# Performance work log

Hardware: AMD Instinct MI355X
Metric: run time of the kernel (lower is better)

The kernel has to match this reference:

```python
import jax, jax.numpy as jnp
from jax import lax
import numpy as np

NODE = 100000
D = 256      # input_dim
H = 256      # hidden_dim
P = 4096     # num paths between the pair
L = 8        # path length (hops)
OUT = 1


def setup_inputs() -> dict:
    key = jax.random.key(0)
    ks = jax.random.split(key, 10)
    s = 1.0 / np.sqrt(H)
    return {
        "embedding": jax.random.normal(ks[0], (NODE, D), jnp.float32) * 0.1,
        "w_ih": jax.random.normal(ks[1], (4 * H, D), jnp.float32) * s,
        "w_hh": jax.random.normal(ks[2], (4 * H, H), jnp.float32) * s,
        "b_ih": jax.random.normal(ks[3], (4 * H,), jnp.float32) * s,
        "b_hh": jax.random.normal(ks[4], (4 * H,), jnp.float32) * s,
        "w_lin": jax.random.normal(ks[5], (OUT, H + 2 * D), jnp.float32) * 0.05,
        "b_lin": jax.random.normal(ks[6], (OUT,), jnp.float32) * 0.05,
        "paths": jax.random.randint(ks[7], (P, L), 0, NODE, jnp.int64),
        "user_id": jax.random.randint(ks[8], (1,), 0, NODE, jnp.int64),
        "item_id": jax.random.randint(ks[9], (1,), 0, NODE, jnp.int64),
    }


def _lstm_final_hidden(x, w_ih, w_hh, b_ih, b_hh):
    # x: [P, L, D] -> final hidden state h_n: [P, H] (PyTorch gate order i,f,g,o)
    p, _, _ = x.shape
    h = x.shape  # noqa (shape comment)
    hidden = w_hh.shape[1]
    b = b_ih + b_hh

    def step(carry, x_t):
        h, c = carry
        gates = x_t @ w_ih.T + h @ w_hh.T + b  # [P, 4H]
        i, f, g, o = jnp.split(gates, 4, axis=-1)
        c = jax.nn.sigmoid(f) * c + jax.nn.sigmoid(i) * jnp.tanh(g)
        h = jax.nn.sigmoid(o) * jnp.tanh(c)
        return (h, c), None

    h0 = jnp.zeros((p, hidden), x.dtype)
    c0 = jnp.zeros((p, hidden), x.dtype)
    (h_n, _), _ = lax.scan(step, (h0, c0), jnp.swapaxes(x, 0, 1))  # scan over L
    return h_n


def reference(embedding, w_ih, w_hh, b_ih, b_hh, w_lin, b_lin, paths, user_id, item_id):
    # Batched version of the per-path loop: embed all paths, one LSTM scan.
    x = embedding[paths]                                   # [P, L, D]
    sum_hidden = _lstm_final_hidden(x, w_ih, w_hh, b_ih, b_hh)  # [P, H] (== stacked h_n)

    # MaxPool2d((1, H)) over hidden dim -> attention logits over paths
    att = jnp.max(sum_hidden, axis=-1, keepdims=True)      # [P, 1]
    att = jax.nn.softmax(att, axis=0)                      # softmax over paths
    path_emb = jnp.sum(sum_hidden * att, axis=0, keepdims=True)  # [1, H]

    user_emb = embedding[user_id]                          # [1, D]
    item_emb = embedding[item_id]                          # [1, D]
    emb = jnp.concatenate([user_emb, item_emb, path_emb], axis=-1)  # [1, 2D+H]
    out = jax.nn.sigmoid(emb @ w_lin.T + b_lin)            # [1, OUT]
    return out
```

## Files before the change

kernel.cpp:

```cpp
#include <hip/hip_runtime.h>
#include <stdint.h>

#define NPATHS 4096
#define LPATH  8
#define DIM    256
#define HID    256

typedef short  short4v __attribute__((ext_vector_type(4)));
typedef short  short8v __attribute__((ext_vector_type(8)));
typedef float  float4v __attribute__((ext_vector_type(4)));

__device__ __forceinline__ unsigned short f2bf(float f) {
    union { float f; uint32_t u; } v; v.f = f;
    uint32_t u = v.u;
    u += 0x7FFFu + ((u >> 16) & 1u);
    return (unsigned short)(u >> 16);
}
__device__ __forceinline__ float bf2f(unsigned short s) {
    return __uint_as_float(((uint32_t)s) << 16);
}
__device__ __forceinline__ float fast_sigmoid(float x) {
    return 1.0f / (1.0f + __expf(-x));
}
__device__ __forceinline__ float fast_tanh(float x) {
    x = fminf(15.0f, fmaxf(-15.0f, x));
    float e = __expf(2.0f * x);
    return (e - 1.0f) / (e + 1.0f);
}
__device__ __forceinline__ unsigned int encf(float f) {
    unsigned int u = __float_as_uint(f);
    return (u & 0x80000000u) ? ~u : (u | 0x80000000u);
}
__device__ __forceinline__ float decf(unsigned int u) {
    return (u & 0x80000000u) ? __uint_as_float(u & 0x7FFFFFFFu) : __uint_as_float(~u);
}

__device__ __forceinline__ void dma16(void* lds, const void* g) {
    typedef const unsigned int __attribute__((address_space(1)))* gp_t;
    typedef unsigned int __attribute__((address_space(3)))* lp_t;
    gp_t gp = reinterpret_cast<gp_t>(reinterpret_cast<uintptr_t>(g));
    lp_t lp = reinterpret_cast<lp_t>(static_cast<unsigned int>(reinterpret_cast<uintptr_t>(lds)));
    __builtin_amdgcn_global_load_lds(gp, lp, 16, 0, 0);
}

__global__ void prep_gather(const float* __restrict__ w_ih, const float* __restrict__ w_hh,
                            const float* __restrict__ b_ih, const float* __restrict__ b_hh,
                            const float* __restrict__ embedding, const int* __restrict__ paths,
                            unsigned short* __restrict__ WfB, float* __restrict__ bias,
                            unsigned int* __restrict__ logits_enc, float* __restrict__ path_emb,
                            unsigned short* __restrict__ Xb) {
    int bid = blockIdx.x;
    if (bid < 512) {
        int gid  = bid * 256 + threadIdx.x;
        int base = gid * 4;
        int j0   = base & 31;
        int unit = (base >> 5) & 255;
        int gkc  = base >> 13;
        int g    = gkc >> 4, kc = gkc & 15;
        int row  = g * 256 + unit;
        int k    = kc * 32 + j0;
        const float* src = (k < DIM) ? (w_ih + (size_t)row * DIM + k)
                                     : (w_hh + (size_t)row * HID + (k - DIM));
        float4 v = *(const float4*)src;
        short4v pk = {(short)f2bf(v.x), (short)f2bf(v.y), (short)f2bf(v.z), (short)f2bf(v.w)};
        *(short4v*)(WfB + base) = pk;
        if (gid < 1024) bias[gid] = b_ih[gid] + b_hh[gid];
        if (gid < NPATHS) logits_enc[gid] = 0u;
        if (gid < 256) path_emb[gid] = 0.0f;
    } else {
        int gid  = (bid - 512) * 256 + threadIdx.x;
        int rowt = gid >> 6;
        int seg  = gid & 63;
        int p    = rowt & (NPATHS - 1);
        int t    = rowt >> 12;
        int node = paths[p * LPATH + t];
        float4 v = *(const float4*)(embedding + (size_t)node * DIM + seg * 4);
        short4v pk = {(short)f2bf(v.x), (short)f2bf(v.y), (short)f2bf(v.z), (short)f2bf(v.w)};
        *(short4v*)(Xb + (size_t)rowt * DIM + seg * 4) = pk;
    }
}

template<bool FIRST, bool LAST>
__global__ __launch_bounds__(256, 1)
void step_kernel(const unsigned short* __restrict__ Xb,
                 const unsigned short* __restrict__ WfB,
                 const float* __restrict__ bias,
                 const unsigned short* __restrict__ h_in,
                 unsigned short* __restrict__ h_out,
                 float* __restrict__ c_g,
                 unsigned int* __restrict__ logits_enc,
                 int t) {
    __shared__ __align__(16) short sA[64 * 512];
    short* hT = sA;

    const int tid   = threadIdx.x;
    const int wave  = tid >> 6;
    const int lane  = tid & 63;
    const int l15   = lane & 15;
    const int quad  = lane >> 4;
    const int blk   = blockIdx.x;
    const int ptile = blk & 63;
    const int utile = blk >> 6;
    const int p0    = ptile * 64;
    const int u0    = utile * 64;

    {
        const char* xpl = (const char*)Xb + ((size_t)t * NPATHS + p0) * 512;
        const char* hpl = (const char*)h_in + (size_t)p0 * 512;
        const char* xl  = xpl + l15 * 512 + quad * 16;
        const char* hl  = hpl + l15 * 512 + quad * 16;
#pragma unroll
        for (int m = 0; m < 16; ++m) {
            int rf = m >> 2, kq = m & 3;
            if (FIRST && kq >= 2) continue;
            int fp = rf * 16 + kq * 4 + wave;
            const char* base = (kq < 2) ? xl : hl;
            int kk = ((kq & 1) * 4 + wave) * 64;
            dma16(sA + fp * 512, base + rf * 8192 + kk);
        }
    }

    short8v Bf[4][16];
    float bb[4];
    const int unit = u0 + wave * 16 + l15;
#pragma unroll
    for (int g = 0; g < 4; ++g) {
        bb[g] = bias[g * 256 + unit];
#pragma unroll
        for (int kc = 0; kc < 16; ++kc)
            Bf[g][kc] = *(const short8v*)(WfB + (((g * 16 + kc) * 256 + unit) * 32 + quad * 8));
    }

    __syncthreads();

    float4v acc[4][4];
    const float4v z4 = {0.0f, 0.0f, 0.0f, 0.0f};
#pragma unroll
    for (int rf = 0; rf < 4; ++rf)
#pragma unroll
        for (int g = 0; g < 4; ++g) acc[rf][g] = z4;

    auto kstep = [&](int kc) {
#pragma unroll
        for (int rf = 0; rf < 4; ++rf) {
            short8v a = *(const short8v*)(sA + ((rf * 16 + kc) << 9) + lane * 8);
#pragma unroll
            for (int g = 0; g < 4; ++g)
                acc[rf][g] = __builtin_amdgcn_mfma_f32_16x16x32_bf16(
                    a, Bf[g][kc], acc[rf][g], 0, 0, 0);
        }
    };
    if (FIRST) {
#pragma unroll
        for (int kc = 0; kc < 8; ++kc) kstep(kc);
    } else {
#pragma unroll
        for (int kc = 0; kc < 16; ++kc) kstep(kc);
    }

    float hv[16];
#pragma unroll
    for (int rf = 0; rf < 4; ++rf) {
#pragma unroll
        for (int r = 0; r < 4; ++r) {
            int row = rf * 16 + quad * 4 + r;
            int idx = rf * 4 + r;
            float iv = acc[rf][0][r] + bb[0];
            float fv = acc[rf][1][r] + bb[1];
            float gv = acc[rf][2][r] + bb[2];
            float ov = acc[rf][3][r] + bb[3];
            size_t coff = (size_t)(p0 + row) * HID + unit;
            float cp = FIRST ? 0.0f : c_g[coff];
            float cn = fast_sigmoid(fv) * cp + fast_sigmoid(iv) * fast_tanh(gv);
            if (!LAST) c_g[coff] = cn;
            hv[idx] = fast_sigmoid(ov) * fast_tanh(cn);
        }
    }

    __syncthreads();
#pragma unroll
    for (int rf = 0; rf < 4; ++rf)
#pragma unroll
        for (int r = 0; r < 4; ++r)
            hT[(rf * 16 + quad * 4 + r) * 72 + wave * 16 + l15] =
                (short)f2bf(hv[rf * 4 + r]);
    __syncthreads();
    {
        unsigned short* hdst = h_out + (size_t)p0 * HID + u0;
#pragma unroll
        for (int i = 0; i < 2; ++i) {
            int cid = i * 256 + tid;
            int row = cid >> 3, seg = cid & 7;
            short8v v = *(const short8v*)(hT + row * 72 + seg * 8);
            *(short8v*)(hdst + (size_t)row * HID + seg * 8) = v;
        }
    }

    if (LAST) {
#pragma unroll
        for (int idx = 0; idx < 16; ++idx) {
            float m = hv[idx];
            m = fmaxf(m, __shfl_xor(m, 1, 64));
            m = fmaxf(m, __shfl_xor(m, 2, 64));
            m = fmaxf(m, __shfl_xor(m, 4, 64));
            m = fmaxf(m, __shfl_xor(m, 8, 64));
            if (l15 == 0) {
                int rf = idx >> 2, r = idx & 3;
                atomicMax(&logits_enc[p0 + rf * 16 + quad * 4 + r], encf(m));
            }
        }
    }
}

__global__ void attn_sum_kernel(const unsigned short* __restrict__ h_final,
                                const unsigned int* __restrict__ enc,
                                float* __restrict__ path_emb) {
    __shared__ float red[256];
    __shared__ float wts[16];
    int tid = threadIdx.x;
    int p0  = blockIdx.x * 16;

    float vals[16];
    float m = -1e30f;
#pragma unroll
    for (int i = 0; i < 16; ++i) {
        vals[i] = decf(enc[i * 256 + tid]);
        m = fmaxf(m, vals[i]);
    }
    red[tid] = m; __syncthreads();
    for (int s = 128; s > 0; s >>= 1) {
        if (tid < s) red[tid] = fmaxf(red[tid], red[tid + s]);
        __syncthreads();
    }
    m = red[0]; __syncthreads();
    float sum = 0.0f;
#pragma unroll
    for (int i = 0; i < 16; ++i) sum += __expf(vals[i] - m);
    red[tid] = sum; __syncthreads();
    for (int s = 128; s > 0; s >>= 1) {
        if (tid < s) red[tid] += red[tid + s];
        __syncthreads();
    }
    if (tid == 0) red[0] = 1.0f / red[0];
    __syncthreads();
    float invZ = red[0];
    if (tid < 16) wts[tid] = __expf(decf(enc[p0 + tid]) - m) * invZ;
    __syncthreads();

    float acc = 0.0f;
#pragma unroll
    for (int j = 0; j < 16; ++j)
        acc += wts[j] * bf2f(h_final[(size_t)(p0 + j) * HID + tid]);
    atomicAdd(&path_emb[tid], acc);
}

__global__ void final_kernel(const float* __restrict__ embedding,
                             const int* __restrict__ user_id,
                             const int* __restrict__ item_id,
                             const float* __restrict__ w_lin,
                             const float* __restrict__ b_lin,
                             const float* __restrict__ path_emb,
                             float* __restrict__ out) {
    __shared__ float red[256];
    int tid = threadIdx.x;
    int u  = user_id[0];
    int it = item_id[0];
    float s = w_lin[tid]       * embedding[(size_t)u  * DIM + tid]
            + w_lin[256 + tid] * embedding[(size_t)it * DIM + tid]
            + w_lin[512 + tid] * path_emb[tid];
    red[tid] = s; __syncthreads();
    for (int st = 128; st > 0; st >>= 1) {
        if (tid < st) red[tid] += red[tid + st];
        __syncthreads();
    }
    if (tid == 0) out[0] = 1.0f / (1.0f + __expf(-(red[0] + b_lin[0])));
}

extern "C" void kernel_launch(void* const* d_in, const int* in_sizes, int n_in,
                              void* d_out, int out_size, void* d_ws, size_t ws_size,
                              hipStream_t stream) {
    const float* embedding = (const float*)d_in[0];
    const float* w_ih      = (const float*)d_in[1];
    const float* w_hh      = (const float*)d_in[2];
    const float* b_ih      = (const float*)d_in[3];
    const float* b_hh      = (const float*)d_in[4];
    const float* w_lin     = (const float*)d_in[5];
    const float* b_lin     = (const float*)d_in[6];
    const int*   paths     = (const int*)d_in[7];
    const int*   user_id   = (const int*)d_in[8];
    const int*   item_id   = (const int*)d_in[9];
    float* outp = (float*)d_out;

    char* ws = (char*)d_ws;
    size_t off = 0;
    auto alloc = [&](size_t n) { void* p = ws + off; off = (off + n + 255) & ~(size_t)255; return p; };
    unsigned short* WfB       = (unsigned short*)alloc((size_t)1024 * 512 * 2);
    float*          bias      = (float*)alloc(1024 * 4);
    unsigned int*   logits_enc= (unsigned int*)alloc(NPATHS * 4);
    float*          path_emb  = (float*)alloc(HID * 4);
    unsigned short* Xb        = (unsigned short*)alloc((size_t)LPATH * NPATHS * DIM * 2);
    unsigned short* h_buf     = (unsigned short*)alloc((size_t)2 * NPATHS * HID * 2);
    float*          c_g       = (float*)alloc((size_t)NPATHS * HID * 4);

    prep_gather<<<8704, 256, 0, stream>>>(w_ih, w_hh, b_ih, b_hh, embedding, paths,
                                          WfB, bias, logits_enc, path_emb, Xb);

    for (int t = 0; t < LPATH; ++t) {
        const unsigned short* hin = h_buf + (size_t)(t & 1) * NPATHS * HID;
        unsigned short*      hout = h_buf + (size_t)((t + 1) & 1) * NPATHS * HID;
        if (t == 0)
            step_kernel<true, false><<<256, 256, 0, stream>>>(Xb, WfB, bias, hin, hout,
                                                              c_g, logits_enc, t);
        else if (t == LPATH - 1)
            step_kernel<false, true><<<256, 256, 0, stream>>>(Xb, WfB, bias, hin, hout,
                                                              c_g, logits_enc, t);
        else
            step_kernel<false, false><<<256, 256, 0, stream>>>(Xb, WfB, bias, hin, hout,
                                                               c_g, logits_enc, t);
    }

    attn_sum_kernel<<<NPATHS / 16, 256, 0, stream>>>(h_buf, logits_enc, path_emb);
    final_kernel<<<1, 256, 0, stream>>>(embedding, user_id, item_id, w_lin, b_lin,
                                        path_emb, outp);
}
```

Baseline: 274.3 us.

## Fuse next-step embedding gather into LSTM step kernel and stream weight fragments

The prep kernel now gathers only the t=0 embeddings. Each step kernel gathers and bf16-packs the embeddings for step t+1 itself, overlapping that latency with the MFMA work and cutting the separate large gather launch. Weight fragments are now streamed four k-chunks ahead instead of all being preloaded into registers. The h_in DMA and c-state loads are issued after the x part starts, so loads overlap compute. In exchange the step kernel grows in complexity, adds an extra barrier, and uses a separate LDS buffer for the transposed h output.

```diff
diff --git a/kernel.cpp b/kernel.cpp
--- a/kernel.cpp
+++ b/kernel.cpp
@@ -41,6 +41,15 @@
     gp_t gp = reinterpret_cast<gp_t>(reinterpret_cast<uintptr_t>(g));
     lp_t lp = reinterpret_cast<lp_t>(static_cast<unsigned int>(reinterpret_cast<uintptr_t>(lds)));
     __builtin_amdgcn_global_load_lds(gp, lp, 16, 0, 0);
+}
+
+__device__ __forceinline__ short8v pack8(float4 a, float4 b) {
+    short8v r;
+    r[0] = (short)f2bf(a.x); r[1] = (short)f2bf(a.y);
+    r[2] = (short)f2bf(a.z); r[3] = (short)f2bf(a.w);
+    r[4] = (short)f2bf(b.x); r[5] = (short)f2bf(b.y);
+    r[6] = (short)f2bf(b.z); r[7] = (short)f2bf(b.w);
+    return r;
 }
 
 __global__ void prep_gather(const float* __restrict__ w_ih, const float* __restrict__ w_hh,
@@ -68,30 +77,35 @@
         if (gid < NPATHS) logits_enc[gid] = 0u;
         if (gid < 256) path_emb[gid] = 0.0f;
     } else {
-        int gid  = (bid - 512) * 256 + threadIdx.x;
-        int rowt = gid >> 6;
-        int seg  = gid & 63;
-        int p    = rowt & (NPATHS - 1);
-        int t    = rowt >> 12;
-        int node = paths[p * LPATH + t];
-        float4 v = *(const float4*)(embedding + (size_t)node * DIM + seg * 4);
-        short4v pk = {(short)f2bf(v.x), (short)f2bf(v.y), (short)f2bf(v.z), (short)f2bf(v.w)};
-        *(short4v*)(Xb + (size_t)rowt * DIM + seg * 4) = pk;
+        int sb   = bid - 512;
+        int row  = (sb & 63) * 64 + (sb >> 6) * 16 + (threadIdx.x >> 4);
+        int c0   = (threadIdx.x & 15) * 16;
+        int node = paths[row * LPATH];
+        const float* src = embedding + (size_t)node * DIM + c0;
+        float4 g0 = *(const float4*)(src + 0);
+        float4 g1 = *(const float4*)(src + 4);
+        float4 g2 = *(const float4*)(src + 8);
+        float4 g3 = *(const float4*)(src + 12);
+        unsigned short* xd = Xb + (size_t)row * 256 + c0;
+        *(short8v*)(xd)     = pack8(g0, g1);
+        *(short8v*)(xd + 8) = pack8(g2, g3);
     }
 }
 
 template<bool FIRST, bool LAST>
 __global__ __launch_bounds__(256, 1)
-void step_kernel(const unsigned short* __restrict__ Xb,
+void step_kernel(unsigned short* __restrict__ Xb,
                  const unsigned short* __restrict__ WfB,
                  const float* __restrict__ bias,
                  const unsigned short* __restrict__ h_in,
                  unsigned short* __restrict__ h_out,
                  float* __restrict__ c_g,
                  unsigned int* __restrict__ logits_enc,
+                 const float* __restrict__ embedding,
+                 const int* __restrict__ paths,
                  int t) {
     __shared__ __align__(16) short sA[64 * 512];
-    short* hT = sA;
+    __shared__ __align__(16) short hTb[64 * 72];
 
     const int tid   = threadIdx.x;
     const int wave  = tid >> 6;
@@ -103,35 +117,61 @@
     const int utile = blk >> 6;
     const int p0    = ptile * 64;
     const int u0    = utile * 64;
+    const int unit  = u0 + wave * 16 + l15;
 
     {
-        const char* xpl = (const char*)Xb + ((size_t)t * NPATHS + p0) * 512;
-        const char* hpl = (const char*)h_in + (size_t)p0 * 512;
-        const char* xl  = xpl + l15 * 512 + quad * 16;
-        const char* hl  = hpl + l15 * 512 + quad * 16;
-#pragma unroll
-        for (int m = 0; m < 16; ++m) {
-            int rf = m >> 2, kq = m & 3;
-            if (FIRST && kq >= 2) continue;
+        const char* xl = (const char*)Xb + ((size_t)t * NPATHS + p0) * 512
+                       + l15 * 512 + quad * 16;
+#pragma unroll
+        for (int m = 0; m < 8; ++m) {
+            int rf = m >> 1, kq = m & 1;
             int fp = rf * 16 + kq * 4 + wave;
-            const char* base = (kq < 2) ? xl : hl;
-            int kk = ((kq & 1) * 4 + wave) * 64;
-            dma16(sA + fp * 512, base + rf * 8192 + kk);
-        }
-    }
-
-    short8v Bf[4][16];
+            dma16(sA + fp * 512, xl + rf * 8192 + (kq * 4 + wave) * 64);
+        }
+    }
+
+    short8v Bs[4][4];
     float bb[4];
-    const int unit = u0 + wave * 16 + l15;
-#pragma unroll
-    for (int g = 0; g < 4; ++g) {
-        bb[g] = bias[g * 256 + unit];
-#pragma unroll
-        for (int kc = 0; kc < 16; ++kc)
-            Bf[g][kc] = *(const short8v*)(WfB + (((g * 16 + kc) * 256 + unit) * 32 + quad * 8));
-    }
-
-    __syncthreads();
+    auto loadB = [&](int kc) {
+#pragma unroll
+        for (int g = 0; g < 4; ++g)
+            Bs[g][kc & 3] = *(const short8v*)(WfB + (((g * 16 + kc) * 256 + unit) * 32 + quad * 8));
+    };
+#pragma unroll
+    for (int g = 0; g < 4; ++g) bb[g] = bias[g * 256 + unit];
+#pragma unroll
+    for (int kc = 0; kc < 4; ++kc) loadB(kc);
+
+    __syncthreads();
+
+    if (!FIRST) {
+        const char* hl = (const char*)h_in + (size_t)p0 * 512 + l15 * 512 + quad * 16;
+#pragma unroll
+        for (int m = 0; m < 8; ++m) {
+            int rf = m >> 1, kq = m & 1;
+            int fp = rf * 16 + 8 + kq * 4 + wave;
+            dma16(sA + fp * 512, hl + rf * 8192 + (kq * 4 + wave) * 64);
+        }
+    }
+
+    float4 gvf[4];
+    int grow = 0;
+    if (!LAST) {
+        grow = p0 + utile * 16 + (tid >> 4);
+        int node = paths[grow * LPATH + (t + 1)];
+        const float* src = embedding + (size_t)node * DIM + (tid & 15) * 16;
+#pragma unroll
+        for (int i = 0; i < 4; ++i) gvf[i] = *(const float4*)(src + i * 4);
+    }
+
+    float cpre[16];
+    if (!FIRST) {
+#pragma unroll
+        for (int rf = 0; rf < 4; ++rf)
+#pragma unroll
+            for (int r = 0; r < 4; ++r)
+                cpre[rf * 4 + r] = c_g[(size_t)(p0 + rf * 16 + quad * 4 + r) * HID + unit];
+    }
 
     float4v acc[4][4];
     const float4v z4 = {0.0f, 0.0f, 0.0f, 0.0f};
@@ -147,15 +187,26 @@
 #pragma unroll
             for (int g = 0; g < 4; ++g)
                 acc[rf][g] = __builtin_amdgcn_mfma_f32_16x16x32_bf16(
-                    a, Bf[g][kc], acc[rf][g], 0, 0, 0);
+                    a, Bs[g][kc & 3], acc[rf][g], 0, 0, 0);
         }
     };
-    if (FIRST) {
-#pragma unroll
-        for (int kc = 0; kc < 8; ++kc) kstep(kc);
-    } else {
-#pragma unroll
-        for (int kc = 0; kc < 16; ++kc) kstep(kc);
+
+#pragma unroll
+    for (int kc = 0; kc < 8; ++kc) {
+        kstep(kc);
+        int nk = kc + 4;
+        if (nk < (FIRST ? 8 : 16)) loadB(nk);
+    }
+
+    __syncthreads();
+
+    if (!FIRST) {
+#pragma unroll
+        for (int kc = 8; kc < 16; ++kc) {
+            kstep(kc);
+            int nk = kc + 4;
+            if (nk < 16) loadB(nk);
+        }
     }
 
     float hv[16];
@@ -167,22 +218,26 @@
             int idx = rf * 4 + r;
             float iv = acc[rf][0][r] + bb[0];
             float fv = acc[rf][1][r] + bb[1];
-            float gv = acc[rf][2][r] + bb[2];
+            float gg = acc[rf][2][r] + bb[2];
             float ov = acc[rf][3][r] + bb[3];
-            size_t coff = (size_t)(p0 + row) * HID + unit;
-            float cp = FIRST ? 0.0f : c_g[coff];
-            float cn = fast_sigmoid(fv) * cp + fast_sigmoid(iv) * fast_tanh(gv);
-            if (!LAST) c_g[coff] = cn;
+            float cp = FIRST ? 0.0f : cpre[idx];
+            float cn = fast_sigmoid(fv) * cp + fast_sigmoid(iv) * fast_tanh(gg);
+            if (!LAST) c_g[(size_t)(p0 + row) * HID + unit] = cn;
             hv[idx] = fast_sigmoid(ov) * fast_tanh(cn);
         }
     }
 
-    __syncthreads();
+    if (!LAST) {
+        unsigned short* xd = Xb + ((size_t)(t + 1) * NPATHS + grow) * 256 + (tid & 15) * 16;
+        *(short8v*)(xd)     = pack8(gvf[0], gvf[1]);
+        *(short8v*)(xd + 8) = pack8(gvf[2], gvf[3]);
+    }
+
 #pragma unroll
     for (int rf = 0; rf < 4; ++rf)
 #pragma unroll
         for (int r = 0; r < 4; ++r)
-            hT[(rf * 16 + quad * 4 + r) * 72 + wave * 16 + l15] =
+            hTb[(rf * 16 + quad * 4 + r) * 72 + wave * 16 + l15] =
                 (short)f2bf(hv[rf * 4 + r]);
     __syncthreads();
     {
@@ -191,7 +246,7 @@
         for (int i = 0; i < 2; ++i) {
             int cid = i * 256 + tid;
             int row = cid >> 3, seg = cid & 7;
-            short8v v = *(const short8v*)(hT + row * 72 + seg * 8);
+            short8v v = *(const short8v*)(hTb + row * 72 + seg * 8);
             *(short8v*)(hdst + (size_t)row * HID + seg * 8) = v;
         }
     }
@@ -302,21 +357,24 @@
     unsigned short* h_buf     = (unsigned short*)alloc((size_t)2 * NPATHS * HID * 2);
     float*          c_g       = (float*)alloc((size_t)NPATHS * HID * 4);
 
-    prep_gather<<<8704, 256, 0, stream>>>(w_ih, w_hh, b_ih, b_hh, embedding, paths,
-                                          WfB, bias, logits_enc, path_emb, Xb);
+    prep_gather<<<768, 256, 0, stream>>>(w_ih, w_hh, b_ih, b_hh, embedding, paths,
+                                         WfB, bias, logits_enc, path_emb, Xb);
 
     for (int t = 0; t < LPATH; ++t) {
         const unsigned short* hin = h_buf + (size_t)(t & 1) * NPATHS * HID;
         unsigned short*      hout = h_buf + (size_t)((t + 1) & 1) * NPATHS * HID;
         if (t == 0)
             step_kernel<true, false><<<256, 256, 0, stream>>>(Xb, WfB, bias, hin, hout,
-                                                              c_g, logits_enc, t);
+                                                              c_g, logits_enc,
+                                                              embedding, paths, t);
         else if (t == LPATH - 1)
             step_kernel<false, true><<<256, 256, 0, stream>>>(Xb, WfB, bias, hin, hout,
-                                                              c_g, logits_enc, t);
+                                                              c_g, logits_enc,
+                                                              embedding, paths, t);
         else
             step_kernel<false, false><<<256, 256, 0, stream>>>(Xb, WfB, bias, hin, hout,
-                                                               c_g, logits_enc, t);
+                                                               c_g, logits_enc,
+                                                               embedding, paths, t);
     }
 
     attn_sum_kernel<<<NPATHS / 16, 256, 0, stream>>>(h_buf, logits_enc, path_emb);
```

New measurement: 266.4 us. 1.03x faster.

## Fuse all LSTM timesteps and the embedding gather into one persistent kernel

Applied to the files above, without the earlier changes.

Replaces the separate gather pass and eight per-timestep launches with a single kernel. Each block owns 16 paths for all 8 steps, keeping the cell state in registers and the hidden state in swizzled LDS, and gathers the next step's embeddings while the current step computes. The final attention reduction and output layer are merged into one kernel that uses a completion counter, and the encoded atomicMax logits are replaced by a direct per-path write. In exchange, every block now streams the whole bf16 weight matrix from global memory on every step, since the weights are no longer kept resident in registers.

```diff
diff --git a/kernel.cpp b/kernel.cpp
--- a/kernel.cpp
+++ b/kernel.cpp
@@ -27,196 +27,212 @@
     float e = __expf(2.0f * x);
     return (e - 1.0f) / (e + 1.0f);
 }
-__device__ __forceinline__ unsigned int encf(float f) {
-    unsigned int u = __float_as_uint(f);
-    return (u & 0x80000000u) ? ~u : (u | 0x80000000u);
-}
-__device__ __forceinline__ float decf(unsigned int u) {
-    return (u & 0x80000000u) ? __uint_as_float(u & 0x7FFFFFFFu) : __uint_as_float(~u);
-}
-
-__device__ __forceinline__ void dma16(void* lds, const void* g) {
-    typedef const unsigned int __attribute__((address_space(1)))* gp_t;
-    typedef unsigned int __attribute__((address_space(3)))* lp_t;
-    gp_t gp = reinterpret_cast<gp_t>(reinterpret_cast<uintptr_t>(g));
-    lp_t lp = reinterpret_cast<lp_t>(static_cast<unsigned int>(reinterpret_cast<uintptr_t>(lds)));
-    __builtin_amdgcn_global_load_lds(gp, lp, 16, 0, 0);
-}
-
-__global__ void prep_gather(const float* __restrict__ w_ih, const float* __restrict__ w_hh,
+
+__global__ void prep_kernel(const float* __restrict__ w_ih, const float* __restrict__ w_hh,
                             const float* __restrict__ b_ih, const float* __restrict__ b_hh,
-                            const float* __restrict__ embedding, const int* __restrict__ paths,
                             unsigned short* __restrict__ WfB, float* __restrict__ bias,
-                            unsigned int* __restrict__ logits_enc, float* __restrict__ path_emb,
-                            unsigned short* __restrict__ Xb) {
-    int bid = blockIdx.x;
-    if (bid < 512) {
-        int gid  = bid * 256 + threadIdx.x;
-        int base = gid * 4;
-        int j0   = base & 31;
-        int unit = (base >> 5) & 255;
-        int gkc  = base >> 13;
-        int g    = gkc >> 4, kc = gkc & 15;
-        int row  = g * 256 + unit;
-        int k    = kc * 32 + j0;
-        const float* src = (k < DIM) ? (w_ih + (size_t)row * DIM + k)
-                                     : (w_hh + (size_t)row * HID + (k - DIM));
-        float4 v = *(const float4*)src;
-        short4v pk = {(short)f2bf(v.x), (short)f2bf(v.y), (short)f2bf(v.z), (short)f2bf(v.w)};
-        *(short4v*)(WfB + base) = pk;
-        if (gid < 1024) bias[gid] = b_ih[gid] + b_hh[gid];
-        if (gid < NPATHS) logits_enc[gid] = 0u;
-        if (gid < 256) path_emb[gid] = 0.0f;
-    } else {
-        int gid  = (bid - 512) * 256 + threadIdx.x;
-        int rowt = gid >> 6;
-        int seg  = gid & 63;
-        int p    = rowt & (NPATHS - 1);
-        int t    = rowt >> 12;
-        int node = paths[p * LPATH + t];
-        float4 v = *(const float4*)(embedding + (size_t)node * DIM + seg * 4);
-        short4v pk = {(short)f2bf(v.x), (short)f2bf(v.y), (short)f2bf(v.z), (short)f2bf(v.w)};
-        *(short4v*)(Xb + (size_t)rowt * DIM + seg * 4) = pk;
-    }
-}
-
-template<bool FIRST, bool LAST>
-__global__ __launch_bounds__(256, 1)
-void step_kernel(const unsigned short* __restrict__ Xb,
-                 const unsigned short* __restrict__ WfB,
-                 const float* __restrict__ bias,
-                 const unsigned short* __restrict__ h_in,
-                 unsigned short* __restrict__ h_out,
-                 float* __restrict__ c_g,
-                 unsigned int* __restrict__ logits_enc,
-                 int t) {
-    __shared__ __align__(16) short sA[64 * 512];
-    short* hT = sA;
-
-    const int tid   = threadIdx.x;
-    const int wave  = tid >> 6;
-    const int lane  = tid & 63;
-    const int l15   = lane & 15;
-    const int quad  = lane >> 4;
-    const int blk   = blockIdx.x;
-    const int ptile = blk & 63;
-    const int utile = blk >> 6;
-    const int p0    = ptile * 64;
-    const int u0    = utile * 64;
+                            float* __restrict__ path_emb, unsigned int* __restrict__ done) {
+    int gid  = blockIdx.x * 256 + threadIdx.x;
+    int base = gid * 4;
+    int j0   = base & 31;
+    int unit = (base >> 5) & 255;
+    int gkc  = base >> 13;
+    int g    = gkc >> 4, kc = gkc & 15;
+    int row  = g * 256 + unit;
+    int k    = kc * 32 + j0;
+    const float* src = (k < DIM) ? (w_ih + (size_t)row * DIM + k)
+                                 : (w_hh + (size_t)row * HID + (k - DIM));
+    float4 v = *(const float4*)src;
+    short4v pk = {(short)f2bf(v.x), (short)f2bf(v.y), (short)f2bf(v.z), (short)f2bf(v.w)};
+    *(short4v*)(WfB + base) = pk;
+    if (gid < 1024) bias[gid] = b_ih[gid] + b_hh[gid];
+    if (gid < 256)  path_emb[gid] = 0.0f;
+    if (gid == 0)   *done = 0u;
+}
+
+__global__ __launch_bounds__(512, 2)
+void mega_kernel(const float* __restrict__ embedding, const int* __restrict__ paths,
+                 const unsigned short* __restrict__ WfB, const float* __restrict__ bias,
+                 unsigned short* __restrict__ h_final, float* __restrict__ logits) {
+    __shared__ __align__(16) short sAx[2][8 * 512];
+    __shared__ __align__(16) short h_lds[16 * 256];
+    __shared__ float red[16 * 8];
+
+    const int tid  = threadIdx.x;
+    const int w    = tid >> 6;
+    const int lane = tid & 63;
+    const int l15  = lane & 15;
+    const int quad = lane >> 4;
+    const int p0   = blockIdx.x * 16;
+    const int unitA = w * 32 + l15;
+    const int unitB = unitA + 16;
+    const int boffA = unitA * 32 + quad * 8;
+    const int boffB = unitB * 32 + quad * 8;
+
+    float bb[4][2];
+#pragma unroll
+    for (int g = 0; g < 4; ++g) {
+        bb[g][0] = bias[g * 256 + unitA];
+        bb[g][1] = bias[g * 256 + unitB];
+    }
 
     {
-        const char* xpl = (const char*)Xb + ((size_t)t * NPATHS + p0) * 512;
-        const char* hpl = (const char*)h_in + (size_t)p0 * 512;
-        const char* xl  = xpl + l15 * 512 + quad * 16;
-        const char* hl  = hpl + l15 * 512 + quad * 16;
-#pragma unroll
-        for (int m = 0; m < 16; ++m) {
-            int rf = m >> 2, kq = m & 3;
-            if (FIRST && kq >= 2) continue;
-            int fp = rf * 16 + kq * 4 + wave;
-            const char* base = (kq < 2) ? xl : hl;
-            int kk = ((kq & 1) * 4 + wave) * 64;
-            dma16(sA + fp * 512, base + rf * 8192 + kk);
-        }
-    }
-
-    short8v Bf[4][16];
-    float bb[4];
-    const int unit = u0 + wave * 16 + l15;
-#pragma unroll
-    for (int g = 0; g < 4; ++g) {
-        bb[g] = bias[g * 256 + unit];
-#pragma unroll
-        for (int kc = 0; kc < 16; ++kc)
-            Bf[g][kc] = *(const short8v*)(WfB + (((g * 16 + kc) * 256 + unit) * 32 + quad * 8));
-    }
-
-    __syncthreads();
-
-    float4v acc[4][4];
-    const float4v z4 = {0.0f, 0.0f, 0.0f, 0.0f};
-#pragma unroll
-    for (int rf = 0; rf < 4; ++rf)
-#pragma unroll
-        for (int g = 0; g < 4; ++g) acc[rf][g] = z4;
-
-    auto kstep = [&](int kc) {
-#pragma unroll
-        for (int rf = 0; rf < 4; ++rf) {
-            short8v a = *(const short8v*)(sA + ((rf * 16 + kc) << 9) + lane * 8);
-#pragma unroll
-            for (int g = 0; g < 4; ++g)
-                acc[rf][g] = __builtin_amdgcn_mfma_f32_16x16x32_bf16(
-                    a, Bf[g][kc], acc[rf][g], 0, 0, 0);
+        int row = tid & 15, k0 = (tid >> 4) * 8;
+        int node = paths[(p0 + row) * LPATH];
+        const float* src = embedding + (size_t)node * DIM + k0;
+        float4 a = *(const float4*)(src);
+        float4 b = *(const float4*)(src + 4);
+        short8v pk;
+        pk[0]=(short)f2bf(a.x); pk[1]=(short)f2bf(a.y); pk[2]=(short)f2bf(a.z); pk[3]=(short)f2bf(a.w);
+        pk[4]=(short)f2bf(b.x); pk[5]=(short)f2bf(b.y); pk[6]=(short)f2bf(b.z); pk[7]=(short)f2bf(b.w);
+        int kc = k0 >> 5, q = (k0 >> 3) & 3;
+        *(short8v*)(&sAx[0][kc * 512 + (q * 16 + row) * 8]) = pk;
+    }
+
+    float cc[4][2] = {{0,0},{0,0},{0,0},{0,0}};
+    __syncthreads();
+
+    short8v Bs[4][4][2];
+    auto loadBk = [&](int kc, int slot) {
+#pragma unroll
+        for (int g = 0; g < 4; ++g) {
+            size_t cb = (size_t)(g * 16 + kc) * 8192;
+            Bs[slot][g][0] = *(const short8v*)(WfB + cb + boffA);
+            Bs[slot][g][1] = *(const short8v*)(WfB + cb + boffB);
         }
     };
-    if (FIRST) {
-#pragma unroll
-        for (int kc = 0; kc < 8; ++kc) kstep(kc);
-    } else {
-#pragma unroll
-        for (int kc = 0; kc < 16; ++kc) kstep(kc);
-    }
-
-    float hv[16];
-#pragma unroll
-    for (int rf = 0; rf < 4; ++rf) {
+
+#pragma unroll 1
+    for (int t = 0; t < LPATH; ++t) {
+        const bool first = (t == 0), last = (t == LPATH - 1);
+
+        float4 gva, gvb;
+        int grow = tid & 15, gk0 = (tid >> 4) * 8;
+        if (!last) {
+            int node = paths[(p0 + grow) * LPATH + t + 1];
+            const float* src = embedding + (size_t)node * DIM + gk0;
+            gva = *(const float4*)(src);
+            gvb = *(const float4*)(src + 4);
+        }
+
+        loadBk(0, 0); loadBk(1, 1); loadBk(2, 2); loadBk(3, 3);
+
+        float4v acc[4][2];
+        const float4v z4 = {0.0f, 0.0f, 0.0f, 0.0f};
+#pragma unroll
+        for (int g = 0; g < 4; ++g) { acc[g][0] = z4; acc[g][1] = z4; }
+
+        const short* sacur = sAx[t & 1];
+
+        auto kstep = [&](int kc, short8v a) {
+#pragma unroll
+            for (int g = 0; g < 4; ++g) {
+                acc[g][0] = __builtin_amdgcn_mfma_f32_16x16x32_bf16(a, Bs[kc & 3][g][0], acc[g][0], 0, 0, 0);
+                acc[g][1] = __builtin_amdgcn_mfma_f32_16x16x32_bf16(a, Bs[kc & 3][g][1], acc[g][1], 0, 0, 0);
+            }
+        };
+
+        if (first) {
+#pragma unroll
+            for (int kc = 0; kc < 8; ++kc) {
+                short8v a = *(const short8v*)(sacur + kc * 512 + lane * 8);
+                kstep(kc, a);
+                if (kc + 4 < 8) loadBk(kc + 4, kc & 3);
+            }
+        } else {
+#pragma unroll
+            for (int kc = 0; kc < 16; ++kc) {
+                short8v a;
+                if (kc < 8) {
+                    a = *(const short8v*)(sacur + kc * 512 + lane * 8);
+                } else {
+                    int kcp = kc - 8;
+                    int cg  = kcp * 4 + quad;
+                    int cgs = cg ^ (l15 & 7);
+                    a = *(const short8v*)(&h_lds[l15 * 256 + cgs * 8]);
+                }
+                kstep(kc, a);
+                if (kc + 4 < 16) loadBk(kc + 4, kc & 3);
+            }
+        }
+
+        if (!last) {
+            short8v pk;
+            pk[0]=(short)f2bf(gva.x); pk[1]=(short)f2bf(gva.y); pk[2]=(short)f2bf(gva.z); pk[3]=(short)f2bf(gva.w);
+            pk[4]=(short)f2bf(gvb.x); pk[5]=(short)f2bf(gvb.y); pk[6]=(short)f2bf(gvb.z); pk[7]=(short)f2bf(gvb.w);
+            int kc = gk0 >> 5, q = (gk0 >> 3) & 3;
+            *(short8v*)(&sAx[(t + 1) & 1][kc * 512 + (q * 16 + grow) * 8]) = pk;
+        }
+
+        float hv[4][2];
 #pragma unroll
         for (int r = 0; r < 4; ++r) {
-            int row = rf * 16 + quad * 4 + r;
-            int idx = rf * 4 + r;
-            float iv = acc[rf][0][r] + bb[0];
-            float fv = acc[rf][1][r] + bb[1];
-            float gv = acc[rf][2][r] + bb[2];
-            float ov = acc[rf][3][r] + bb[3];
-            size_t coff = (size_t)(p0 + row) * HID + unit;
-            float cp = FIRST ? 0.0f : c_g[coff];
-            float cn = fast_sigmoid(fv) * cp + fast_sigmoid(iv) * fast_tanh(gv);
-            if (!LAST) c_g[coff] = cn;
-            hv[idx] = fast_sigmoid(ov) * fast_tanh(cn);
-        }
-    }
-
-    __syncthreads();
-#pragma unroll
-    for (int rf = 0; rf < 4; ++rf)
-#pragma unroll
-        for (int r = 0; r < 4; ++r)
-            hT[(rf * 16 + quad * 4 + r) * 72 + wave * 16 + l15] =
-                (short)f2bf(hv[rf * 4 + r]);
-    __syncthreads();
+#pragma unroll
+            for (int e = 0; e < 2; ++e) {
+                float iv = acc[0][e][r] + bb[0][e];
+                float fv = acc[1][e][r] + bb[1][e];
+                float gg = acc[2][e][r] + bb[2][e];
+                float ov = acc[3][e][r] + bb[3][e];
+                float cn = fast_sigmoid(fv) * cc[r][e] + fast_sigmoid(iv) * fast_tanh(gg);
+                cc[r][e] = cn;
+                hv[r][e] = fast_sigmoid(ov) * fast_tanh(cn);
+            }
+        }
+
+        __syncthreads();
+
+#pragma unroll
+        for (int r = 0; r < 4; ++r) {
+            int pr = quad * 4 + r;
+#pragma unroll
+            for (int e = 0; e < 2; ++e) {
+                int u   = (e == 0) ? unitA : unitB;
+                int cgs = (u >> 3) ^ (pr & 7);
+                h_lds[pr * 256 + cgs * 8 + (u & 7)] = (short)f2bf(hv[r][e]);
+            }
+        }
+
+        if (last) {
+#pragma unroll
+            for (int r = 0; r < 4; ++r) {
+                float m = fmaxf(hv[r][0], hv[r][1]);
+                m = fmaxf(m, __shfl_xor(m, 1, 64));
+                m = fmaxf(m, __shfl_xor(m, 2, 64));
+                m = fmaxf(m, __shfl_xor(m, 4, 64));
+                m = fmaxf(m, __shfl_xor(m, 8, 64));
+                if (l15 == 0) red[(quad * 4 + r) * 8 + w] = m;
+            }
+        }
+        __syncthreads();
+    }
+
+    if (tid < 16) {
+        float m = red[tid * 8];
+#pragma unroll
+        for (int j = 1; j < 8; ++j) m = fmaxf(m, red[tid * 8 + j]);
+        logits[p0 + tid] = m;
+    }
     {
-        unsigned short* hdst = h_out + (size_t)p0 * HID + u0;
-#pragma unroll
-        for (int i = 0; i < 2; ++i) {
-            int cid = i * 256 + tid;
-            int row = cid >> 3, seg = cid & 7;
-            short8v v = *(const short8v*)(hT + row * 72 + seg * 8);
-            *(short8v*)(hdst + (size_t)row * HID + seg * 8) = v;
-        }
-    }
-
-    if (LAST) {
-#pragma unroll
-        for (int idx = 0; idx < 16; ++idx) {
-            float m = hv[idx];
-            m = fmaxf(m, __shfl_xor(m, 1, 64));
-            m = fmaxf(m, __shfl_xor(m, 2, 64));
-            m = fmaxf(m, __shfl_xor(m, 4, 64));
-            m = fmaxf(m, __shfl_xor(m, 8, 64));
-            if (l15 == 0) {
-                int rf = idx >> 2, r = idx & 3;
-                atomicMax(&logits_enc[p0 + rf * 16 + quad * 4 + r], encf(m));
-            }
-        }
-    }
-}
-
-__global__ void attn_sum_kernel(const unsigned short* __restrict__ h_final,
-                                const unsigned int* __restrict__ enc,
-                                float* __restrict__ path_emb) {
+        int row = tid >> 5, i5 = tid & 31;
+        int cgs = i5 ^ (row & 7);
+        short8v v = *(const short8v*)(&h_lds[row * 256 + cgs * 8]);
+        *(short8v*)(h_final + (size_t)(p0 + row) * HID + (size_t)i5 * 8) = v;
+    }
+}
+
+__global__ void attn_final_kernel(const unsigned short* __restrict__ h_final,
+                                  const float* __restrict__ logits,
+                                  float* __restrict__ path_emb,
+                                  unsigned int* __restrict__ done,
+                                  const float* __restrict__ embedding,
+                                  const int* __restrict__ user_id,
+                                  const int* __restrict__ item_id,
+                                  const float* __restrict__ w_lin,
+                                  const float* __restrict__ b_lin,
+                                  float* __restrict__ out) {
     __shared__ float red[256];
     __shared__ float wts[16];
+    __shared__ int lastf;
     int tid = threadIdx.x;
     int p0  = blockIdx.x * 16;
 
@@ -224,7 +240,7 @@
     float m = -1e30f;
 #pragma unroll
     for (int i = 0; i < 16; ++i) {
-        vals[i] = decf(enc[i * 256 + tid]);
+        vals[i] = logits[i * 256 + tid];
         m = fmaxf(m, vals[i]);
     }
     red[tid] = m; __syncthreads();
@@ -244,7 +260,7 @@
     if (tid == 0) red[0] = 1.0f / red[0];
     __syncthreads();
     float invZ = red[0];
-    if (tid < 16) wts[tid] = __expf(decf(enc[p0 + tid]) - m) * invZ;
+    if (tid < 16) wts[tid] = __expf(logits[p0 + tid] - m) * invZ;
     __syncthreads();
 
     float acc = 0.0f;
@@ -252,28 +268,30 @@
     for (int j = 0; j < 16; ++j)
         acc += wts[j] * bf2f(h_final[(size_t)(p0 + j) * HID + tid]);
     atomicAdd(&path_emb[tid], acc);
-}
-
-__global__ void final_kernel(const float* __restrict__ embedding,
-                             const int* __restrict__ user_id,
-                             const int* __restrict__ item_id,
-                             const float* __restrict__ w_lin,
-                             const float* __restrict__ b_lin,
-                             const float* __restrict__ path_emb,
-                             float* __restrict__ out) {
-    __shared__ float red[256];
-    int tid = threadIdx.x;
-    int u  = user_id[0];
-    int it = item_id[0];
-    float s = w_lin[tid]       * embedding[(size_t)u  * DIM + tid]
-            + w_lin[256 + tid] * embedding[(size_t)it * DIM + tid]
-            + w_lin[512 + tid] * path_emb[tid];
-    red[tid] = s; __syncthreads();
-    for (int st = 128; st > 0; st >>= 1) {
-        if (tid < st) red[tid] += red[tid + st];
-        __syncthreads();
-    }
-    if (tid == 0) out[0] = 1.0f / (1.0f + __expf(-(red[0] + b_lin[0])));
+
+    __threadfence();
+    __syncthreads();
+    if (tid == 0) {
+        unsigned int old = atomicAdd(done, 1u);
+        lastf = (old == 255u) ? 1 : 0;
+    }
+    __syncthreads();
+    if (lastf) {
+        __threadfence();
+        float pe = __hip_atomic_load(&path_emb[tid], __ATOMIC_RELAXED,
+                                     __HIP_MEMORY_SCOPE_AGENT);
+        int u  = user_id[0];
+        int it = item_id[0];
+        float s = w_lin[tid]       * embedding[(size_t)u  * DIM + tid]
+                + w_lin[256 + tid] * embedding[(size_t)it * DIM + tid]
+                + w_lin[512 + tid] * pe;
+        red[tid] = s; __syncthreads();
+        for (int st = 128; st > 0; st >>= 1) {
+            if (tid < st) red[tid] += red[tid + st];
+            __syncthreads();
+        }
+        if (tid == 0) out[0] = 1.0f / (1.0f + __expf(-(red[0] + b_lin[0])));
+    }
 }
 
 extern "C" void kernel_launch(void* const* d_in, const int* in_sizes, int n_in,
@@ -294,32 +312,20 @@
     char* ws = (char*)d_ws;
     size_t off = 0;
     auto alloc = [&](size_t n) { void* p = ws + off; off = (off + n + 255) & ~(size_t)255; return p; };
-    unsigned short* WfB       = (unsigned short*)alloc((size_t)1024 * 512 * 2);
-    float*          bias      = (float*)alloc(1024 * 4);
-    unsigned int*   logits_enc= (unsigned int*)alloc(NPATHS * 4);
-    float*          path_emb  = (float*)alloc(HID * 4);
-    unsigned short* Xb        = (unsigned short*)alloc((size_t)LPATH * NPATHS * DIM * 2);
-    unsigned short* h_buf     = (unsigned short*)alloc((size_t)2 * NPATHS * HID * 2);
-    float*          c_g       = (float*)alloc((size_t)NPATHS * HID * 4);
-
-    prep_gather<<<8704, 256, 0, stream>>>(w_ih, w_hh, b_ih, b_hh, embedding, paths,
-                                          WfB, bias, logits_enc, path_emb, Xb);
-
-    for (int t = 0; t < LPATH; ++t) {
-        const unsigned short* hin = h_buf + (size_t)(t & 1) * NPATHS * HID;
-        unsigned short*      hout = h_buf + (size_t)((t + 1) & 1) * NPATHS * HID;
-        if (t == 0)
-            step_kernel<true, false><<<256, 256, 0, stream>>>(Xb, WfB, bias, hin, hout,
-                                                              c_g, logits_enc, t);
-        else if (t == LPATH - 1)
-            step_kernel<false, true><<<256, 256, 0, stream>>>(Xb, WfB, bias, hin, hout,
-                                                              c_g, logits_enc, t);
-        else
-            step_kernel<false, false><<<256, 256, 0, stream>>>(Xb, WfB, bias, hin, hout,
-                                                               c_g, logits_enc, t);
-    }
-
-    attn_sum_kernel<<<NPATHS / 16, 256, 0, stream>>>(h_buf, logits_enc, path_emb);
-    final_kernel<<<1, 256, 0, stream>>>(embedding, user_id, item_id, w_lin, b_lin,
-                                        path_emb, outp);
-}
+    unsigned short* WfB      = (unsigned short*)alloc((size_t)1024 * 512 * 2);
+    float*          bias     = (float*)alloc(1024 * 4);
+    float*          path_emb = (float*)alloc(HID * 4);
+    float*          logits   = (float*)alloc(NPATHS * 4);
+    unsigned short* h_final  = (unsigned short*)alloc((size_t)NPATHS * HID * 2);
+    unsigned int*   done     = (unsigned int*)alloc(4);
+
+    prep_kernel<<<512, 256, 0, stream>>>(w_ih, w_hh, b_ih, b_hh, WfB, bias,
+                                         path_emb, done);
+
+    mega_kernel<<<256, 512, 0, stream>>>(embedding, paths, WfB, bias,
+                                         h_final, logits);
+
+    attn_final_kernel<<<256, 256, 0, stream>>>(h_final, logits, path_emb, done,
+                                               embedding, user_id, item_id,
+                                               w_lin, b_lin, outp);
+}
```

Result: slower. 529.5 us (+93.1%).
